# Kernel tuning notes

Hardware: AMD Instinct MI355X
Metric: run time of the kernel (lower is better)

The kernel has to match this reference:

```python
import jax, jax.numpy as jnp
import numpy as np

GRID = 32          # latent grid points per dim
N_OUT = 16384      # output query points
BATCH = 2
C = 256            # projection_channels (latent hidden width)
D = 3              # gno_coord_dim
OUT_CH = 4         # out_channels
RADIUS = 0.045     # gno_radius


def _radius_neighbors(x, y, r):
    """Radius ball search: for each query x_i find all y_j with ||x_i-y_j||<=r.
    Returns (nb_index, out_index) edge lists, sorted by query (CSR order)."""
    r2 = np.float32(r * r)
    nb_idx, out_idx = [], []
    for s in range(0, x.shape[0], 512):  # chunk to bound memory
        d2 = ((x[s:s + 512, None, :] - y[None, :, :]) ** 2).sum(-1)
        oi, yi = np.nonzero(d2 <= r2)
        out_idx.append((oi + s).astype(np.int32))
        nb_idx.append(yi.astype(np.int32))
    return np.concatenate(nb_idx), np.concatenate(out_idx)


def setup_inputs() -> dict:
    key = jax.random.key(0)
    ks = jax.random.split(key, 8)
    # latent queries: regular grid on [0,1]^3
    g = np.linspace(0.0, 1.0, GRID, dtype=np.float32)
    gx, gy, gz = np.meshgrid(g, g, g, indexing="ij")
    grid = np.stack([gx, gy, gz], axis=-1)               # (G,G,G,3)
    latent_queries = jnp.asarray(grid[None])             # (1,G,G,G,3)
    output_queries = jax.random.uniform(ks[0], (1, N_OUT, D), dtype=jnp.float32)
    nb_idx, out_idx = _radius_neighbors(np.asarray(output_queries[0]),
                                        grid.reshape(-1, D), RADIUS)
    latent_embed = jax.random.normal(ks[1], (BATCH, GRID, GRID, GRID, C), dtype=jnp.float32)

    def lin(k, fi, fo):
        kw, kb = jax.random.split(k)
        W = jax.random.normal(kw, (fi, fo), dtype=jnp.float32) / np.sqrt(fi).astype(np.float32)
        b = jax.random.normal(kb, (fo,), dtype=jnp.float32) * 0.01
        return W, b

    W1, b1 = lin(ks[2], 2 * D, 512)
    W2, b2 = lin(ks[3], 512, 256)
    W3, b3 = lin(ks[4], 256, C)
    Wp, bp = lin(ks[5], C, OUT_CH)
    return {"latent_embed": latent_embed, "latent_queries": latent_queries,
            "output_queries": output_queries,
            "nb_index": jnp.asarray(nb_idx), "out_index": jnp.asarray(out_idx),
            "W1": W1, "b1": b1, "W2": W2, "b2": b2, "W3": W3, "b3": b3,
            "Wp": Wp, "bp": bp}


def reference(latent_embed, latent_queries, output_queries, nb_index, out_index,
              W1, b1, W2, b2, W3, b3, Wp, bp):
    y = latent_queries[0].reshape(-1, latent_queries.shape[-1])   # (n_in, d) grid coords
    x = output_queries[0]                                         # (n_out, d)
    n_out = x.shape[0]
    b = latent_embed.shape[0]
    f_y = latent_embed.reshape(b, -1, latent_embed.shape[-1])     # (b, n_in, c)

    # per-edge kernel MLP on concat(y_j, x_i) -- 'linear' transform type
    agg = jnp.concatenate([y[nb_index], x[out_index]], axis=-1)   # (E, 2d)
    h = jax.nn.gelu(agg @ W1 + b1, approximate=False)             # (E, 512)
    h = jax.nn.gelu(h @ W2 + b2, approximate=False)               # (E, 256)
    k = h @ W3 + b3                                               # (E, c) kernel values

    # k(x_i, y_j) * f(y_j), then mean-reduce over each neighborhood
    msg = k[None, :, :] * f_y[:, nb_index, :]                     # (b, E, c)
    sums = jax.vmap(lambda m: jax.ops.segment_sum(m, out_index, num_segments=n_out))(msg)
    cnt = jax.ops.segment_sum(jnp.ones(nb_index.shape[0], dtype=k.dtype),
                              out_index, num_segments=n_out)
    mean = sums / jnp.maximum(cnt, 1.0)[None, :, None]            # (b, n_out, c)

    # pointwise projection (single Linear, no nonlinearity)
    return mean @ Wp + bp                                         # (b, n_out, out_ch)
```

## Files before the change

kernel.cpp:

```cpp
#include <hip/hip_runtime.h>
#include <math.h>

#define NGRID 32768
#define NOUT  16384
#define CCH   256
#define H1DIM 512
#define TE    64
#define NTHR  512

typedef _Float16 f16x8 __attribute__((ext_vector_type(8)));
typedef float    f32x16 __attribute__((ext_vector_type(16)));

__device__ __forceinline__ unsigned short f32_to_f16_bits(float v) {
    _Float16 h = (_Float16)v;
    return __builtin_bit_cast(unsigned short, h);
}

__device__ __forceinline__ float gelu_fast(float x) {
    float ax = fabsf(x) * 0.70710678118654752f;
    float t  = __builtin_amdgcn_rcpf(fmaf(0.3275911f, ax, 1.0f));
    float p  = fmaf(fmaf(fmaf(fmaf(1.061405429f, t, -1.453152027f), t, 1.421413741f), t,
                         -0.284496736f), t, 0.254829592f) * t;
    float e  = __expf(-ax * ax);
    float er = fmaf(-p, e, 1.0f);
    er = (x >= 0.0f) ? er : -er;
    return 0.5f * x * (1.0f + er);
}

__global__ __launch_bounds__(256) void gino_pack_kernel(
    const float* __restrict__ W2, const float* __restrict__ W3,
    unsigned short* __restrict__ W2F, unsigned short* __restrict__ W3F)
{
    int idx = blockIdx.x * 256 + threadIdx.x;
    if (idx < 32 * 8 * 64) {
        int l = idx & 63, g = (idx >> 6) & 7, ks = idx >> 9;
        int ch = g * 32 + (l & 31);
        int k0 = ks * 16 + (l >> 5) * 8;
        unsigned int u[4];
        #pragma unroll
        for (int p = 0; p < 4; ++p) {
            unsigned int lo = f32_to_f16_bits(W2[(k0 + 2 * p) * CCH + ch]);
            unsigned int hh = f32_to_f16_bits(W2[(k0 + 2 * p + 1) * CCH + ch]);
            u[p] = lo | (hh << 16);
        }
        *(uint4*)(W2F + idx * 8) = make_uint4(u[0], u[1], u[2], u[3]);
    } else if (idx < 32 * 8 * 64 + 16 * 8 * 64) {
        int i2 = idx - 32 * 8 * 64;
        int l = i2 & 63, g = (i2 >> 6) & 7, ks = i2 >> 9;
        int ch = g * 32 + (l & 31);
        int k0 = ks * 16 + (l >> 5) * 8;
        unsigned int u[4];
        #pragma unroll
        for (int p = 0; p < 4; ++p) {
            unsigned int lo = f32_to_f16_bits(W3[(k0 + 2 * p) * CCH + ch]);
            unsigned int hh = f32_to_f16_bits(W3[(k0 + 2 * p + 1) * CCH + ch]);
            u[p] = lo | (hh << 16);
        }
        *(uint4*)(W3F + i2 * 8) = make_uint4(u[0], u[1], u[2], u[3]);
    }
}

__global__ __launch_bounds__(NTHR, 4) void gino_edge_kernel(
    const float* __restrict__ latent_embed,
    const float* __restrict__ latent_queries,
    const float* __restrict__ output_queries,
    const int*   __restrict__ nb_index,
    const int*   __restrict__ out_index,
    const float* __restrict__ W1, const float* __restrict__ b1,
    const float* __restrict__ b2, const float* __restrict__ b3,
    const unsigned short* __restrict__ W2F,
    const unsigned short* __restrict__ W3F,
    const float* __restrict__ Wp,
    float* __restrict__ sums, float* __restrict__ cnt, int E)
{
    __shared__ __align__(16) unsigned char s_h1[TE * 256];
    __shared__ __align__(16) unsigned char s_h2[TE * 512];
    __shared__ float s_agg[TE][8];
    __shared__ float s_pm[TE][8];
    __shared__ int s_nb[TE], s_oi[TE], s_valid[TE];

    const int tid = threadIdx.x;
    const int e0  = blockIdx.x * TE;

    ((float*)s_pm)[tid] = 0.0f;
    if (tid < TE) {
        int e     = e0 + tid;
        int valid = (e < E) ? 1 : 0;
        int ec    = valid ? e : (E - 1);
        int nb    = nb_index[ec];
        int oi    = out_index[ec];
        s_nb[tid] = nb; s_oi[tid] = oi; s_valid[tid] = valid;
        s_agg[tid][0] = latent_queries[nb * 3 + 0];
        s_agg[tid][1] = latent_queries[nb * 3 + 1];
        s_agg[tid][2] = latent_queries[nb * 3 + 2];
        s_agg[tid][3] = output_queries[oi * 3 + 0];
        s_agg[tid][4] = output_queries[oi * 3 + 1];
        s_agg[tid][5] = output_queries[oi * 3 + 2];
        if (valid) atomicAdd(&cnt[oi], 1.0f);
    }
    __syncthreads();

    const int l  = tid & 63;
    const int w  = tid >> 6;
    const int le = l & 31;
    const int hi = l >> 5;
    const unsigned bsw1 = (unsigned)(le & 15) << 4;
    const unsigned bsw2 = (unsigned)(le & 31) << 4;

    f32x16 acc0 = {}, acc1 = {};

    #pragma unroll
    for (int c = 0; c < 4; ++c) {
        const unsigned short* gw = W2F + (size_t)(c * 8) * 4096 + w * 512 + l * 8;
        f16x8 a[8];
        #pragma unroll
        for (int ks = 0; ks < 8; ++ks)
            a[ks] = *(const f16x8*)(gw + (size_t)ks * 4096);
        __builtin_amdgcn_sched_barrier(0);

        {
            const int col = c * 128 + l * 2;
            float w0[6], w1v[6];
            #pragma unroll
            for (int i = 0; i < 6; ++i) {
                float2 t2 = *(const float2*)(W1 + i * H1DIM + col);
                w0[i] = t2.x; w1v[i] = t2.y;
            }
            float2 bb = *(const float2*)(b1 + col);
            #pragma unroll
            for (int ee = 0; ee < 8; ++ee) {
                int e = w * 8 + ee;
                float v0 = bb.x, v1 = bb.y;
                #pragma unroll
                for (int i = 0; i < 6; ++i) {
                    float av = s_agg[e][i];
                    v0 = fmaf(av, w0[i], v0);
                    v1 = fmaf(av, w1v[i], v1);
                }
                unsigned u = (unsigned)f32_to_f16_bits(gelu_fast(v0)) |
                             ((unsigned)f32_to_f16_bits(gelu_fast(v1)) << 16);
                *(unsigned*)(s_h1 + e * 256 + (((unsigned)(l * 4)) ^ (((unsigned)(e & 15)) << 4))) = u;
            }
        }
        __syncthreads();

        #pragma unroll
        for (int ks = 0; ks < 8; ++ks) {
            f16x8 b0 = *(const f16x8*)(s_h1 + le * 256 +
                           (((unsigned)(ks * 32 + hi * 16)) ^ bsw1));
            f16x8 b1f = *(const f16x8*)(s_h1 + (32 + le) * 256 +
                           (((unsigned)(ks * 32 + hi * 16)) ^ bsw1));
            acc0 = __builtin_amdgcn_mfma_f32_32x32x16_f16(a[ks], b0,  acc0, 0, 0, 0);
            acc1 = __builtin_amdgcn_mfma_f32_32x32x16_f16(a[ks], b1f, acc1, 0, 0, 0);
        }
        __syncthreads();
    }

    const unsigned short* gw3 = W3F + w * 512 + l * 8;
    f16x8 a3[16];
    #pragma unroll
    for (int ks = 0; ks < 16; ++ks)
        a3[ks] = *(const f16x8*)(gw3 + (size_t)ks * 4096);
    __builtin_amdgcn_sched_barrier(0);

    #pragma unroll
    for (int t = 0; t < 2; ++t) {
        int erow = t * 32 + le;
        unsigned esw = (unsigned)(erow & 31) << 4;
        #pragma unroll
        for (int q = 0; q < 4; ++q) {
            int ch0 = w * 32 + q * 8 + hi * 4;
            float4 bb = *(const float4*)(b2 + ch0);
            float v0 = (t ? acc1[q * 4 + 0] : acc0[q * 4 + 0]) + bb.x;
            float v1 = (t ? acc1[q * 4 + 1] : acc0[q * 4 + 1]) + bb.y;
            float v2 = (t ? acc1[q * 4 + 2] : acc0[q * 4 + 2]) + bb.z;
            float v3 = (t ? acc1[q * 4 + 3] : acc0[q * 4 + 3]) + bb.w;
            unsigned int u0 = f32_to_f16_bits(gelu_fast(v0)) |
                              ((unsigned)f32_to_f16_bits(gelu_fast(v1)) << 16);
            unsigned int u1 = f32_to_f16_bits(gelu_fast(v2)) |
                              ((unsigned)f32_to_f16_bits(gelu_fast(v3)) << 16);
            *(uint2*)(s_h2 + erow * 512 + (((unsigned)(ch0 * 2)) ^ esw)) = make_uint2(u0, u1);
        }
    }
    __syncthreads();

    f32x16 kc0 = {}, kc1 = {};
    #pragma unroll
    for (int ks = 0; ks < 16; ++ks) {
        f16x8 b0 = *(const f16x8*)(s_h2 + le * 512 +
                       (((unsigned)(ks * 32 + hi * 16)) ^ bsw2));
        f16x8 b1f = *(const f16x8*)(s_h2 + (32 + le) * 512 +
                       (((unsigned)(ks * 32 + hi * 16)) ^ bsw2));
        kc0 = __builtin_amdgcn_mfma_f32_32x32x16_f16(a3[ks], b0,  kc0, 0, 0, 0);
        kc1 = __builtin_amdgcn_mfma_f32_32x32x16_f16(a3[ks], b1f, kc1, 0, 0, 0);
    }

    #pragma unroll
    for (int t = 0; t < 2; ++t) {
        int e  = t * 32 + le;
        int nb = s_nb[e];
        const float* fb0 = latent_embed + (size_t)nb * CCH;
        const float* fb1 = latent_embed + ((size_t)NGRID + nb) * CCH;
        float pm[8] = {0.f, 0.f, 0.f, 0.f, 0.f, 0.f, 0.f, 0.f};
        #pragma unroll
        for (int q = 0; q < 4; ++q) {
            int ch0 = w * 32 + q * 8 + hi * 4;
            float4 bb = *(const float4*)(b3 + ch0);
            float kv0 = (t ? kc1[q * 4 + 0] : kc0[q * 4 + 0]) + bb.x;
            float kv1 = (t ? kc1[q * 4 + 1] : kc0[q * 4 + 1]) + bb.y;
            float kv2 = (t ? kc1[q * 4 + 2] : kc0[q * 4 + 2]) + bb.z;
            float kv3 = (t ? kc1[q * 4 + 3] : kc0[q * 4 + 3]) + bb.w;
            float4 f0 = *(const float4*)(fb0 + ch0);
            float4 f1 = *(const float4*)(fb1 + ch0);
            float4 wp0 = *(const float4*)(Wp + (ch0 + 0) * 4);
            float4 wp1 = *(const float4*)(Wp + (ch0 + 1) * 4);
            float4 wp2 = *(const float4*)(Wp + (ch0 + 2) * 4);
            float4 wp3 = *(const float4*)(Wp + (ch0 + 3) * 4);
            float t0 = kv0 * f0.x, t1 = kv1 * f0.y, t2v = kv2 * f0.z, t3 = kv3 * f0.w;
            pm[0] = fmaf(t0, wp0.x, fmaf(t1, wp1.x, fmaf(t2v, wp2.x, fmaf(t3, wp3.x, pm[0]))));
            pm[1] = fmaf(t0, wp0.y, fmaf(t1, wp1.y, fmaf(t2v, wp2.y, fmaf(t3, wp3.y, pm[1]))));
            pm[2] = fmaf(t0, wp0.z, fmaf(t1, wp1.z, fmaf(t2v, wp2.z, fmaf(t3, wp3.z, pm[2]))));
            pm[3] = fmaf(t0, wp0.w, fmaf(t1, wp1.w, fmaf(t2v, wp2.w, fmaf(t3, wp3.w, pm[3]))));
            float s0 = kv0 * f1.x, s1 = kv1 * f1.y, s2 = kv2 * f1.z, s3 = kv3 * f1.w;
            pm[4] = fmaf(s0, wp0.x, fmaf(s1, wp1.x, fmaf(s2, wp2.x, fmaf(s3, wp3.x, pm[4]))));
            pm[5] = fmaf(s0, wp0.y, fmaf(s1, wp1.y, fmaf(s2, wp2.y, fmaf(s3, wp3.y, pm[5]))));
            pm[6] = fmaf(s0, wp0.z, fmaf(s1, wp1.z, fmaf(s2, wp2.z, fmaf(s3, wp3.z, pm[6]))));
            pm[7] = fmaf(s0, wp0.w, fmaf(s1, wp1.w, fmaf(s2, wp2.w, fmaf(s3, wp3.w, pm[7]))));
        }
        #pragma unroll
        for (int v = 0; v < 8; ++v) pm[v] += __shfl_xor(pm[v], 32);
        if (hi == 0) {
            #pragma unroll
            for (int v = 0; v < 8; ++v) atomicAdd(&s_pm[e][v], pm[v]);
        }
    }
    __syncthreads();

    {
        int el = tid >> 3;
        int v  = tid & 7;
        if (s_valid[el]) {
            int b  = v >> 2;
            int oc = v & 3;
            atomicAdd(&sums[((size_t)b * NOUT + s_oi[el]) * 4 + oc], s_pm[el][v]);
        }
    }
}

__global__ __launch_bounds__(256) void gino_finalize_kernel(
    const float* __restrict__ sums,
    const float* __restrict__ cnt,
    const float* __restrict__ bp,
    float* __restrict__ out)
{
    int idx = blockIdx.x * 256 + threadIdx.x;
    if (idx >= 2 * NOUT * 4) return;
    int oc = idx & 3;
    int i  = (idx >> 2) & (NOUT - 1);
    float c = fmaxf(cnt[i], 1.0f);
    out[idx] = sums[idx] / c + bp[oc];
}

extern "C" void kernel_launch(void* const* d_in, const int* in_sizes, int n_in,
                              void* d_out, int out_size, void* d_ws, size_t ws_size,
                              hipStream_t stream) {
    const float* latent_embed   = (const float*)d_in[0];
    const float* latent_queries = (const float*)d_in[1];
    const float* output_queries = (const float*)d_in[2];
    const int*   nb_index       = (const int*)d_in[3];
    const int*   out_index      = (const int*)d_in[4];
    const float* W1 = (const float*)d_in[5];
    const float* b1 = (const float*)d_in[6];
    const float* W2 = (const float*)d_in[7];
    const float* b2 = (const float*)d_in[8];
    const float* W3 = (const float*)d_in[9];
    const float* b3 = (const float*)d_in[10];
    const float* Wp = (const float*)d_in[11];
    const float* bp = (const float*)d_in[12];

    const int E = in_sizes[3];

    float* sums = (float*)d_ws;
    float* cnt  = sums + 2 * NOUT * 4;
    unsigned short* W2F = (unsigned short*)(cnt + NOUT);
    unsigned short* W3F = W2F + 32 * 8 * 64 * 8;

    hipMemsetAsync(d_ws, 0, (size_t)(2 * NOUT * 4 + NOUT) * sizeof(float), stream);

    gino_pack_kernel<<<(32 * 8 * 64 + 16 * 8 * 64 + 255) / 256, 256, 0, stream>>>(
        W2, W3, W2F, W3F);

    int nblk = (E + TE - 1) / TE;
    gino_edge_kernel<<<nblk, NTHR, 0, stream>>>(
        latent_embed, latent_queries, output_queries, nb_index, out_index,
        W1, b1, b2, b3, W2F, W3F, Wp, sums, cnt, E);

    gino_finalize_kernel<<<(2 * NOUT * 4 + 255) / 256, 256, 0, stream>>>(
        sums, cnt, bp, (float*)d_out);
}
```

Baseline: 262.1 us.

## Prefetch latent features before final MFMA and remap blocks for XCD locality

Block indices are remapped so consecutive edge tiles land on the same XCD, which is meant to improve L2 reuse of the gathered latent rows, since CSR-sorted edges share neighbors. The latent_embed gathers for the first 32 edges are issued before the W3 MFMA loop and those for the second 32 right after it, with sched_barriers, so global load latency overlaps the matrix work. The cost is more live VGPRs (two sets of 8 float4), which could reduce occupancy.

```diff
diff --git a/kernel.cpp b/kernel.cpp
--- a/kernel.cpp
+++ b/kernel.cpp
@@ -80,7 +80,11 @@
     __shared__ int s_nb[TE], s_oi[TE], s_valid[TE];
 
     const int tid = threadIdx.x;
-    const int e0  = blockIdx.x * TE;
+
+    int bid = blockIdx.x, nwg = gridDim.x;
+    int xc = bid & 7, qq = nwg >> 3, rr = nwg & 7;
+    int sb = (xc < rr ? xc * (qq + 1) : rr * (qq + 1) + (xc - rr) * qq) + (bid >> 3);
+    const int e0 = sb * TE;
 
     ((float*)s_pm)[tid] = 0.0f;
     if (tid < TE) {
@@ -106,6 +110,7 @@
     const int hi = l >> 5;
     const unsigned bsw1 = (unsigned)(le & 15) << 4;
     const unsigned bsw2 = (unsigned)(le & 31) << 4;
+    const int ch_base = w * 32 + hi * 4;
 
     f32x16 acc0 = {}, acc1 = {};
 
@@ -184,6 +189,19 @@
     }
     __syncthreads();
 
+    const int nb0 = s_nb[le], nb1 = s_nb[32 + le];
+    float4 fA[8];
+    {
+        const float* f00 = latent_embed + (size_t)nb0 * CCH;
+        const float* f01 = latent_embed + ((size_t)NGRID + nb0) * CCH;
+        #pragma unroll
+        for (int q = 0; q < 4; ++q) {
+            fA[q]     = *(const float4*)(f00 + ch_base + q * 8);
+            fA[4 + q] = *(const float4*)(f01 + ch_base + q * 8);
+        }
+    }
+    __builtin_amdgcn_sched_barrier(0);
+
     f32x16 kc0 = {}, kc1 = {};
     #pragma unroll
     for (int ks = 0; ks < 16; ++ks) {
@@ -195,45 +213,56 @@
         kc1 = __builtin_amdgcn_mfma_f32_32x32x16_f16(a3[ks], b1f, kc1, 0, 0, 0);
     }
 
-    #pragma unroll
-    for (int t = 0; t < 2; ++t) {
-        int e  = t * 32 + le;
-        int nb = s_nb[e];
-        const float* fb0 = latent_embed + (size_t)nb * CCH;
-        const float* fb1 = latent_embed + ((size_t)NGRID + nb) * CCH;
-        float pm[8] = {0.f, 0.f, 0.f, 0.f, 0.f, 0.f, 0.f, 0.f};
+    float4 fB[8];
+    {
+        const float* f10 = latent_embed + (size_t)nb1 * CCH;
+        const float* f11 = latent_embed + ((size_t)NGRID + nb1) * CCH;
         #pragma unroll
         for (int q = 0; q < 4; ++q) {
-            int ch0 = w * 32 + q * 8 + hi * 4;
-            float4 bb = *(const float4*)(b3 + ch0);
-            float kv0 = (t ? kc1[q * 4 + 0] : kc0[q * 4 + 0]) + bb.x;
-            float kv1 = (t ? kc1[q * 4 + 1] : kc0[q * 4 + 1]) + bb.y;
-            float kv2 = (t ? kc1[q * 4 + 2] : kc0[q * 4 + 2]) + bb.z;
-            float kv3 = (t ? kc1[q * 4 + 3] : kc0[q * 4 + 3]) + bb.w;
-            float4 f0 = *(const float4*)(fb0 + ch0);
-            float4 f1 = *(const float4*)(fb1 + ch0);
-            float4 wp0 = *(const float4*)(Wp + (ch0 + 0) * 4);
-            float4 wp1 = *(const float4*)(Wp + (ch0 + 1) * 4);
-            float4 wp2 = *(const float4*)(Wp + (ch0 + 2) * 4);
-            float4 wp3 = *(const float4*)(Wp + (ch0 + 3) * 4);
-            float t0 = kv0 * f0.x, t1 = kv1 * f0.y, t2v = kv2 * f0.z, t3 = kv3 * f0.w;
-            pm[0] = fmaf(t0, wp0.x, fmaf(t1, wp1.x, fmaf(t2v, wp2.x, fmaf(t3, wp3.x, pm[0]))));
-            pm[1] = fmaf(t0, wp0.y, fmaf(t1, wp1.y, fmaf(t2v, wp2.y, fmaf(t3, wp3.y, pm[1]))));
-            pm[2] = fmaf(t0, wp0.z, fmaf(t1, wp1.z, fmaf(t2v, wp2.z, fmaf(t3, wp3.z, pm[2]))));
-            pm[3] = fmaf(t0, wp0.w, fmaf(t1, wp1.w, fmaf(t2v, wp2.w, fmaf(t3, wp3.w, pm[3]))));
-            float s0 = kv0 * f1.x, s1 = kv1 * f1.y, s2 = kv2 * f1.z, s3 = kv3 * f1.w;
-            pm[4] = fmaf(s0, wp0.x, fmaf(s1, wp1.x, fmaf(s2, wp2.x, fmaf(s3, wp3.x, pm[4]))));
-            pm[5] = fmaf(s0, wp0.y, fmaf(s1, wp1.y, fmaf(s2, wp2.y, fmaf(s3, wp3.y, pm[5]))));
-            pm[6] = fmaf(s0, wp0.z, fmaf(s1, wp1.z, fmaf(s2, wp2.z, fmaf(s3, wp3.z, pm[6]))));
-            pm[7] = fmaf(s0, wp0.w, fmaf(s1, wp1.w, fmaf(s2, wp2.w, fmaf(s3, wp3.w, pm[7]))));
-        }
-        #pragma unroll
-        for (int v = 0; v < 8; ++v) pm[v] += __shfl_xor(pm[v], 32);
-        if (hi == 0) {
-            #pragma unroll
-            for (int v = 0; v < 8; ++v) atomicAdd(&s_pm[e][v], pm[v]);
-        }
-    }
+            fB[q]     = *(const float4*)(f10 + ch_base + q * 8);
+            fB[4 + q] = *(const float4*)(f11 + ch_base + q * 8);
+        }
+    }
+    __builtin_amdgcn_sched_barrier(0);
+
+    #define TILE_DOT(FF, KC, EIDX) do {                                            \
+        float pm[8] = {0.f, 0.f, 0.f, 0.f, 0.f, 0.f, 0.f, 0.f};                    \
+        _Pragma("unroll")                                                          \
+        for (int q = 0; q < 4; ++q) {                                              \
+            int ch0 = ch_base + q * 8;                                             \
+            float4 bb = *(const float4*)(b3 + ch0);                                \
+            float kv0 = KC[q * 4 + 0] + bb.x;                                      \
+            float kv1 = KC[q * 4 + 1] + bb.y;                                      \
+            float kv2 = KC[q * 4 + 2] + bb.z;                                      \
+            float kv3 = KC[q * 4 + 3] + bb.w;                                      \
+            float4 f0 = FF[q];                                                     \
+            float4 f1 = FF[4 + q];                                                 \
+            float4 wp0 = *(const float4*)(Wp + (ch0 + 0) * 4);                     \
+            float4 wp1 = *(const float4*)(Wp + (ch0 + 1) * 4);                     \
+            float4 wp2 = *(const float4*)(Wp + (ch0 + 2) * 4);                     \
+            float4 wp3 = *(const float4*)(Wp + (ch0 + 3) * 4);                     \
+            float t0 = kv0 * f0.x, t1 = kv1 * f0.y, t2v = kv2 * f0.z, t3 = kv3 * f0.w; \
+            pm[0] = fmaf(t0, wp0.x, fmaf(t1, wp1.x, fmaf(t2v, wp2.x, fmaf(t3, wp3.x, pm[0])))); \
+            pm[1] = fmaf(t0, wp0.y, fmaf(t1, wp1.y, fmaf(t2v, wp2.y, fmaf(t3, wp3.y, pm[1])))); \
+            pm[2] = fmaf(t0, wp0.z, fmaf(t1, wp1.z, fmaf(t2v, wp2.z, fmaf(t3, wp3.z, pm[2])))); \
+            pm[3] = fmaf(t0, wp0.w, fmaf(t1, wp1.w, fmaf(t2v, wp2.w, fmaf(t3, wp3.w, pm[3])))); \
+            float s0 = kv0 * f1.x, s1 = kv1 * f1.y, s2 = kv2 * f1.z, s3 = kv3 * f1.w; \
+            pm[4] = fmaf(s0, wp0.x, fmaf(s1, wp1.x, fmaf(s2, wp2.x, fmaf(s3, wp3.x, pm[4])))); \
+            pm[5] = fmaf(s0, wp0.y, fmaf(s1, wp1.y, fmaf(s2, wp2.y, fmaf(s3, wp3.y, pm[5])))); \
+            pm[6] = fmaf(s0, wp0.z, fmaf(s1, wp1.z, fmaf(s2, wp2.z, fmaf(s3, wp3.z, pm[6])))); \
+            pm[7] = fmaf(s0, wp0.w, fmaf(s1, wp1.w, fmaf(s2, wp2.w, fmaf(s3, wp3.w, pm[7])))); \
+        }                                                                          \
+        _Pragma("unroll")                                                          \
+        for (int v = 0; v < 8; ++v) pm[v] += __shfl_xor(pm[v], 32);                \
+        if (hi == 0) {                                                             \
+            _Pragma("unroll")                                                      \
+            for (int v = 0; v < 8; ++v) atomicAdd(&s_pm[EIDX][v], pm[v]);          \
+        }                                                                          \
+    } while (0)
+
+    TILE_DOT(fA, kc0, le);
+    TILE_DOT(fB, kc1, (32 + le));
+    #undef TILE_DOT
     __syncthreads();
 
     {
```

After: 428.6 us. +63.5%, slower.

## Halve edge tile, give each wave two weight groups, add fp16 embedding copy

Applied to the files above, without the earlier changes.

The edge tile drops from 64 to 32 edges per 256-thread block. Each wave now covers two channel groups of 32 edges instead of one group of 64, so every MFMA reuses the same LDS B operand against two weight fragments. The W3 fragment loads and the latent_embed gathers are split into stages placed between MFMA chunks to hide latency. When the workspace is large enough, an extra pass converts latent_embed to fp16 so the gathers move half the bytes. That costs an additional full-tensor conversion kernel and some precision loss, and the smaller tile means more blocks each reloading W2/W3.

```diff
diff --git a/kernel.cpp b/kernel.cpp
--- a/kernel.cpp
+++ b/kernel.cpp
@@ -5,8 +5,8 @@
 #define NOUT  16384
 #define CCH   256
 #define H1DIM 512
-#define TE    64
-#define NTHR  512
+#define TE    32
+#define NTHR  256
 
 typedef _Float16 f16x8 __attribute__((ext_vector_type(8)));
 typedef float    f32x16 __attribute__((ext_vector_type(16)));
@@ -14,6 +14,12 @@
 __device__ __forceinline__ unsigned short f32_to_f16_bits(float v) {
     _Float16 h = (_Float16)v;
     return __builtin_bit_cast(unsigned short, h);
+}
+__device__ __forceinline__ float h2l(unsigned u) {
+    return (float)__builtin_bit_cast(_Float16, (unsigned short)(u & 0xffff));
+}
+__device__ __forceinline__ float h2h(unsigned u) {
+    return (float)__builtin_bit_cast(_Float16, (unsigned short)(u >> 16));
 }
 
 __device__ __forceinline__ float gelu_fast(float x) {
@@ -60,8 +66,23 @@
     }
 }
 
+__global__ __launch_bounds__(256) void gino_embed_f16_kernel(
+    const float* __restrict__ in, unsigned short* __restrict__ out)
+{
+    int i = (blockIdx.x * 256 + threadIdx.x) * 8;
+    float4 a = *(const float4*)(in + i);
+    float4 b = *(const float4*)(in + i + 4);
+    unsigned u0 = (unsigned)f32_to_f16_bits(a.x) | ((unsigned)f32_to_f16_bits(a.y) << 16);
+    unsigned u1 = (unsigned)f32_to_f16_bits(a.z) | ((unsigned)f32_to_f16_bits(a.w) << 16);
+    unsigned u2 = (unsigned)f32_to_f16_bits(b.x) | ((unsigned)f32_to_f16_bits(b.y) << 16);
+    unsigned u3 = (unsigned)f32_to_f16_bits(b.z) | ((unsigned)f32_to_f16_bits(b.w) << 16);
+    *(uint4*)(out + i) = make_uint4(u0, u1, u2, u3);
+}
+
+template <int F16E>
 __global__ __launch_bounds__(NTHR, 4) void gino_edge_kernel(
     const float* __restrict__ latent_embed,
+    const unsigned short* __restrict__ fembed,
     const float* __restrict__ latent_queries,
     const float* __restrict__ output_queries,
     const int*   __restrict__ nb_index,
@@ -106,16 +127,20 @@
     const int hi = l >> 5;
     const unsigned bsw1 = (unsigned)(le & 15) << 4;
     const unsigned bsw2 = (unsigned)(le & 31) << 4;
+    const int g0 = w, g1 = w + 4;
 
     f32x16 acc0 = {}, acc1 = {};
 
     #pragma unroll
     for (int c = 0; c < 4; ++c) {
-        const unsigned short* gw = W2F + (size_t)(c * 8) * 4096 + w * 512 + l * 8;
-        f16x8 a[8];
-        #pragma unroll
-        for (int ks = 0; ks < 8; ++ks)
-            a[ks] = *(const f16x8*)(gw + (size_t)ks * 4096);
+        const unsigned short* gw0 = W2F + (size_t)(c * 8) * 4096 + g0 * 512 + l * 8;
+        const unsigned short* gw1 = W2F + (size_t)(c * 8) * 4096 + g1 * 512 + l * 8;
+        f16x8 aP[8], aQ[8];
+        #pragma unroll
+        for (int ks = 0; ks < 8; ++ks) {
+            aP[ks] = *(const f16x8*)(gw0 + (size_t)ks * 4096);
+            aQ[ks] = *(const f16x8*)(gw1 + (size_t)ks * 4096);
+        }
         __builtin_amdgcn_sched_barrier(0);
 
         {
@@ -146,92 +171,156 @@
 
         #pragma unroll
         for (int ks = 0; ks < 8; ++ks) {
-            f16x8 b0 = *(const f16x8*)(s_h1 + le * 256 +
-                           (((unsigned)(ks * 32 + hi * 16)) ^ bsw1));
-            f16x8 b1f = *(const f16x8*)(s_h1 + (32 + le) * 256 +
-                           (((unsigned)(ks * 32 + hi * 16)) ^ bsw1));
-            acc0 = __builtin_amdgcn_mfma_f32_32x32x16_f16(a[ks], b0,  acc0, 0, 0, 0);
-            acc1 = __builtin_amdgcn_mfma_f32_32x32x16_f16(a[ks], b1f, acc1, 0, 0, 0);
+            f16x8 b = *(const f16x8*)(s_h1 + le * 256 +
+                          (((unsigned)(ks * 32 + hi * 16)) ^ bsw1));
+            acc0 = __builtin_amdgcn_mfma_f32_32x32x16_f16(aP[ks], b, acc0, 0, 0, 0);
+            acc1 = __builtin_amdgcn_mfma_f32_32x32x16_f16(aQ[ks], b, acc1, 0, 0, 0);
         }
         __syncthreads();
     }
 
-    const unsigned short* gw3 = W3F + w * 512 + l * 8;
-    f16x8 a3[16];
-    #pragma unroll
-    for (int ks = 0; ks < 16; ++ks)
-        a3[ks] = *(const f16x8*)(gw3 + (size_t)ks * 4096);
+    f16x8 a3P[8], a3Q[8];
+    #pragma unroll
+    for (int ks = 0; ks < 8; ++ks) {
+        a3P[ks] = *(const f16x8*)(W3F + (size_t)ks * 4096 + g0 * 512 + l * 8);
+        a3Q[ks] = *(const f16x8*)(W3F + (size_t)(8 + ks) * 4096 + g0 * 512 + l * 8);
+    }
     __builtin_amdgcn_sched_barrier(0);
 
     #pragma unroll
-    for (int t = 0; t < 2; ++t) {
-        int erow = t * 32 + le;
-        unsigned esw = (unsigned)(erow & 31) << 4;
+    for (int gi = 0; gi < 2; ++gi) {
+        int g = w + gi * 4;
         #pragma unroll
         for (int q = 0; q < 4; ++q) {
-            int ch0 = w * 32 + q * 8 + hi * 4;
+            int ch0 = g * 32 + q * 8 + hi * 4;
             float4 bb = *(const float4*)(b2 + ch0);
-            float v0 = (t ? acc1[q * 4 + 0] : acc0[q * 4 + 0]) + bb.x;
-            float v1 = (t ? acc1[q * 4 + 1] : acc0[q * 4 + 1]) + bb.y;
-            float v2 = (t ? acc1[q * 4 + 2] : acc0[q * 4 + 2]) + bb.z;
-            float v3 = (t ? acc1[q * 4 + 3] : acc0[q * 4 + 3]) + bb.w;
-            unsigned int u0 = f32_to_f16_bits(gelu_fast(v0)) |
-                              ((unsigned)f32_to_f16_bits(gelu_fast(v1)) << 16);
-            unsigned int u1 = f32_to_f16_bits(gelu_fast(v2)) |
-                              ((unsigned)f32_to_f16_bits(gelu_fast(v3)) << 16);
-            *(uint2*)(s_h2 + erow * 512 + (((unsigned)(ch0 * 2)) ^ esw)) = make_uint2(u0, u1);
+            float v0 = (gi ? acc1[q * 4 + 0] : acc0[q * 4 + 0]) + bb.x;
+            float v1 = (gi ? acc1[q * 4 + 1] : acc0[q * 4 + 1]) + bb.y;
+            float v2 = (gi ? acc1[q * 4 + 2] : acc0[q * 4 + 2]) + bb.z;
+            float v3 = (gi ? acc1[q * 4 + 3] : acc0[q * 4 + 3]) + bb.w;
+            unsigned u0 = f32_to_f16_bits(gelu_fast(v0)) |
+                          ((unsigned)f32_to_f16_bits(gelu_fast(v1)) << 16);
+            unsigned u1 = f32_to_f16_bits(gelu_fast(v2)) |
+                          ((unsigned)f32_to_f16_bits(gelu_fast(v3)) << 16);
+            *(uint2*)(s_h2 + le * 512 + (((unsigned)(ch0 * 2)) ^ bsw2)) = make_uint2(u0, u1);
         }
     }
     __syncthreads();
 
+    const int nb0 = s_nb[le];
+    const int cb0 = g0 * 32 + hi * 4, cb1 = g1 * 32 + hi * 4;
+    float4 fF0[8]; uint2 fH0[8];
+    if constexpr (F16E) {
+        const unsigned short* fp = fembed + (size_t)nb0 * CCH;
+        #pragma unroll
+        for (int q = 0; q < 4; ++q) {
+            fH0[q]     = *(const uint2*)(fp + cb0 + q * 8);
+            fH0[4 + q] = *(const uint2*)(fp + (size_t)NGRID * CCH + cb0 + q * 8);
+        }
+    } else {
+        const float* fp = latent_embed + (size_t)nb0 * CCH;
+        #pragma unroll
+        for (int q = 0; q < 4; ++q) {
+            fF0[q]     = *(const float4*)(fp + cb0 + q * 8);
+            fF0[4 + q] = *(const float4*)(fp + (size_t)NGRID * CCH + cb0 + q * 8);
+        }
+    }
+    __builtin_amdgcn_sched_barrier(0);
+
     f32x16 kc0 = {}, kc1 = {};
     #pragma unroll
-    for (int ks = 0; ks < 16; ++ks) {
-        f16x8 b0 = *(const f16x8*)(s_h2 + le * 512 +
-                       (((unsigned)(ks * 32 + hi * 16)) ^ bsw2));
-        f16x8 b1f = *(const f16x8*)(s_h2 + (32 + le) * 512 +
-                       (((unsigned)(ks * 32 + hi * 16)) ^ bsw2));
-        kc0 = __builtin_amdgcn_mfma_f32_32x32x16_f16(a3[ks], b0,  kc0, 0, 0, 0);
-        kc1 = __builtin_amdgcn_mfma_f32_32x32x16_f16(a3[ks], b1f, kc1, 0, 0, 0);
-    }
-
-    #pragma unroll
-    for (int t = 0; t < 2; ++t) {
-        int e  = t * 32 + le;
-        int nb = s_nb[e];
-        const float* fb0 = latent_embed + (size_t)nb * CCH;
-        const float* fb1 = latent_embed + ((size_t)NGRID + nb) * CCH;
+    for (int ks = 0; ks < 8; ++ks) {
+        f16x8 b = *(const f16x8*)(s_h2 + le * 512 +
+                      (((unsigned)(ks * 32 + hi * 16)) ^ bsw2));
+        kc0 = __builtin_amdgcn_mfma_f32_32x32x16_f16(a3P[ks], b, kc0, 0, 0, 0);
+    }
+    #pragma unroll
+    for (int ks = 0; ks < 8; ++ks)
+        a3P[ks] = *(const f16x8*)(W3F + (size_t)ks * 4096 + g1 * 512 + l * 8);
+    float4 fF1[8]; uint2 fH1[8];
+    if constexpr (F16E) {
+        const unsigned short* fp = fembed + (size_t)nb0 * CCH;
+        #pragma unroll
+        for (int q = 0; q < 4; ++q) {
+            fH1[q]     = *(const uint2*)(fp + cb1 + q * 8);
+            fH1[4 + q] = *(const uint2*)(fp + (size_t)NGRID * CCH + cb1 + q * 8);
+        }
+    } else {
+        const float* fp = latent_embed + (size_t)nb0 * CCH;
+        #pragma unroll
+        for (int q = 0; q < 4; ++q) {
+            fF1[q]     = *(const float4*)(fp + cb1 + q * 8);
+            fF1[4 + q] = *(const float4*)(fp + (size_t)NGRID * CCH + cb1 + q * 8);
+        }
+    }
+    __builtin_amdgcn_sched_barrier(0);
+    #pragma unroll
+    for (int ks = 0; ks < 8; ++ks) {
+        f16x8 b = *(const f16x8*)(s_h2 + le * 512 +
+                      (((unsigned)((8 + ks) * 32 + hi * 16)) ^ bsw2));
+        kc0 = __builtin_amdgcn_mfma_f32_32x32x16_f16(a3Q[ks], b, kc0, 0, 0, 0);
+    }
+    #pragma unroll
+    for (int ks = 0; ks < 8; ++ks)
+        a3Q[ks] = *(const f16x8*)(W3F + (size_t)(8 + ks) * 4096 + g1 * 512 + l * 8);
+    __builtin_amdgcn_sched_barrier(0);
+    #pragma unroll
+    for (int ks = 0; ks < 8; ++ks) {
+        f16x8 b = *(const f16x8*)(s_h2 + le * 512 +
+                      (((unsigned)(ks * 32 + hi * 16)) ^ bsw2));
+        kc1 = __builtin_amdgcn_mfma_f32_32x32x16_f16(a3P[ks], b, kc1, 0, 0, 0);
+    }
+    #pragma unroll
+    for (int ks = 0; ks < 8; ++ks) {
+        f16x8 b = *(const f16x8*)(s_h2 + le * 512 +
+                      (((unsigned)((8 + ks) * 32 + hi * 16)) ^ bsw2));
+        kc1 = __builtin_amdgcn_mfma_f32_32x32x16_f16(a3Q[ks], b, kc1, 0, 0, 0);
+    }
+
+    {
         float pm[8] = {0.f, 0.f, 0.f, 0.f, 0.f, 0.f, 0.f, 0.f};
         #pragma unroll
-        for (int q = 0; q < 4; ++q) {
-            int ch0 = w * 32 + q * 8 + hi * 4;
-            float4 bb = *(const float4*)(b3 + ch0);
-            float kv0 = (t ? kc1[q * 4 + 0] : kc0[q * 4 + 0]) + bb.x;
-            float kv1 = (t ? kc1[q * 4 + 1] : kc0[q * 4 + 1]) + bb.y;
-            float kv2 = (t ? kc1[q * 4 + 2] : kc0[q * 4 + 2]) + bb.z;
-            float kv3 = (t ? kc1[q * 4 + 3] : kc0[q * 4 + 3]) + bb.w;
-            float4 f0 = *(const float4*)(fb0 + ch0);
-            float4 f1 = *(const float4*)(fb1 + ch0);
-            float4 wp0 = *(const float4*)(Wp + (ch0 + 0) * 4);
-            float4 wp1 = *(const float4*)(Wp + (ch0 + 1) * 4);
-            float4 wp2 = *(const float4*)(Wp + (ch0 + 2) * 4);
-            float4 wp3 = *(const float4*)(Wp + (ch0 + 3) * 4);
-            float t0 = kv0 * f0.x, t1 = kv1 * f0.y, t2v = kv2 * f0.z, t3 = kv3 * f0.w;
-            pm[0] = fmaf(t0, wp0.x, fmaf(t1, wp1.x, fmaf(t2v, wp2.x, fmaf(t3, wp3.x, pm[0]))));
-            pm[1] = fmaf(t0, wp0.y, fmaf(t1, wp1.y, fmaf(t2v, wp2.y, fmaf(t3, wp3.y, pm[1]))));
-            pm[2] = fmaf(t0, wp0.z, fmaf(t1, wp1.z, fmaf(t2v, wp2.z, fmaf(t3, wp3.z, pm[2]))));
-            pm[3] = fmaf(t0, wp0.w, fmaf(t1, wp1.w, fmaf(t2v, wp2.w, fmaf(t3, wp3.w, pm[3]))));
-            float s0 = kv0 * f1.x, s1 = kv1 * f1.y, s2 = kv2 * f1.z, s3 = kv3 * f1.w;
-            pm[4] = fmaf(s0, wp0.x, fmaf(s1, wp1.x, fmaf(s2, wp2.x, fmaf(s3, wp3.x, pm[4]))));
-            pm[5] = fmaf(s0, wp0.y, fmaf(s1, wp1.y, fmaf(s2, wp2.y, fmaf(s3, wp3.y, pm[5]))));
-            pm[6] = fmaf(s0, wp0.z, fmaf(s1, wp1.z, fmaf(s2, wp2.z, fmaf(s3, wp3.z, pm[6]))));
-            pm[7] = fmaf(s0, wp0.w, fmaf(s1, wp1.w, fmaf(s2, wp2.w, fmaf(s3, wp3.w, pm[7]))));
+        for (int gi = 0; gi < 2; ++gi) {
+            int cb = gi ? cb1 : cb0;
+            #pragma unroll
+            for (int q = 0; q < 4; ++q) {
+                int ch0 = cb + q * 8;
+                float4 bb = *(const float4*)(b3 + ch0);
+                float kv0 = (gi ? kc1[q * 4 + 0] : kc0[q * 4 + 0]) + bb.x;
+                float kv1 = (gi ? kc1[q * 4 + 1] : kc0[q * 4 + 1]) + bb.y;
+                float kv2 = (gi ? kc1[q * 4 + 2] : kc0[q * 4 + 2]) + bb.z;
+                float kv3 = (gi ? kc1[q * 4 + 3] : kc0[q * 4 + 3]) + bb.w;
+                float4 f0, f1;
+                if constexpr (F16E) {
+                    uint2 u0 = gi ? fH1[q] : fH0[q];
+                    uint2 u1 = gi ? fH1[4 + q] : fH0[4 + q];
+                    f0 = make_float4(h2l(u0.x), h2h(u0.x), h2l(u0.y), h2h(u0.y));
+                    f1 = make_float4(h2l(u1.x), h2h(u1.x), h2l(u1.y), h2h(u1.y));
+                } else {
+                    f0 = gi ? fF1[q] : fF0[q];
+                    f1 = gi ? fF1[4 + q] : fF0[4 + q];
+                }
+                float4 wp0 = *(const float4*)(Wp + (ch0 + 0) * 4);
+                float4 wp1 = *(const float4*)(Wp + (ch0 + 1) * 4);
+                float4 wp2 = *(const float4*)(Wp + (ch0 + 2) * 4);
+                float4 wp3 = *(const float4*)(Wp + (ch0 + 3) * 4);
+                float t0 = kv0 * f0.x, t1 = kv1 * f0.y, t2v = kv2 * f0.z, t3 = kv3 * f0.w;
+                pm[0] = fmaf(t0, wp0.x, fmaf(t1, wp1.x, fmaf(t2v, wp2.x, fmaf(t3, wp3.x, pm[0]))));
+                pm[1] = fmaf(t0, wp0.y, fmaf(t1, wp1.y, fmaf(t2v, wp2.y, fmaf(t3, wp3.y, pm[1]))));
+                pm[2] = fmaf(t0, wp0.z, fmaf(t1, wp1.z, fmaf(t2v, wp2.z, fmaf(t3, wp3.z, pm[2]))));
+                pm[3] = fmaf(t0, wp0.w, fmaf(t1, wp1.w, fmaf(t2v, wp2.w, fmaf(t3, wp3.w, pm[3]))));
+                float s0 = kv0 * f1.x, s1 = kv1 * f1.y, s2 = kv2 * f1.z, s3 = kv3 * f1.w;
+                pm[4] = fmaf(s0, wp0.x, fmaf(s1, wp1.x, fmaf(s2, wp2.x, fmaf(s3, wp3.x, pm[4]))));
+                pm[5] = fmaf(s0, wp0.y, fmaf(s1, wp1.y, fmaf(s2, wp2.y, fmaf(s3, wp3.y, pm[5]))));
+                pm[6] = fmaf(s0, wp0.z, fmaf(s1, wp1.z, fmaf(s2, wp2.z, fmaf(s3, wp3.z, pm[6]))));
+                pm[7] = fmaf(s0, wp0.w, fmaf(s1, wp1.w, fmaf(s2, wp2.w, fmaf(s3, wp3.w, pm[7]))));
+            }
         }
         #pragma unroll
         for (int v = 0; v < 8; ++v) pm[v] += __shfl_xor(pm[v], 32);
         if (hi == 0) {
             #pragma unroll
-            for (int v = 0; v < 8; ++v) atomicAdd(&s_pm[e][v], pm[v]);
+            for (int v = 0; v < 8; ++v) atomicAdd(&s_pm[le][v], pm[v]);
         }
     }
     __syncthreads();
@@ -284,6 +373,10 @@
     float* cnt  = sums + 2 * NOUT * 4;
     unsigned short* W2F = (unsigned short*)(cnt + NOUT);
     unsigned short* W3F = W2F + 32 * 8 * 64 * 8;
+    unsigned short* fembed = W3F + 16 * 8 * 64 * 8;
+    const size_t base_bytes = (size_t)((char*)fembed - (char*)d_ws);
+    const size_t femb_bytes = (size_t)2 * NGRID * CCH * 2;
+    const bool use_f16 = ws_size >= base_bytes + femb_bytes;
 
     hipMemsetAsync(d_ws, 0, (size_t)(2 * NOUT * 4 + NOUT) * sizeof(float), stream);
 
@@ -291,9 +384,17 @@
         W2, W3, W2F, W3F);
 
     int nblk = (E + TE - 1) / TE;
-    gino_edge_kernel<<<nblk, NTHR, 0, stream>>>(
-        latent_embed, latent_queries, output_queries, nb_index, out_index,
-        W1, b1, b2, b3, W2F, W3F, Wp, sums, cnt, E);
+    if (use_f16) {
+        gino_embed_f16_kernel<<<(2 * NGRID * CCH / 8 + 255) / 256, 256, 0, stream>>>(
+            latent_embed, fembed);
+        gino_edge_kernel<1><<<nblk, NTHR, 0, stream>>>(
+            latent_embed, fembed, latent_queries, output_queries, nb_index, out_index,
+            W1, b1, b2, b3, W2F, W3F, Wp, sums, cnt, E);
+    } else {
+        gino_edge_kernel<0><<<nblk, NTHR, 0, stream>>>(
+            latent_embed, (const unsigned short*)nullptr, latent_queries, output_queries,
+            nb_index, out_index, W1, b1, b2, b3, W2F, W3F, Wp, sums, cnt, E);
+    }
 
     gino_finalize_kernel<<<(2 * NOUT * 4 + 255) / 256, 256, 0, stream>>>(
         sums, cnt, bp, (float*)d_out);
```

Result: slower. 468.2 us (+78.6%).
